# Optimization experiments

Hardware: AMD Instinct MI355X
Metric: run time of the kernel (lower is better)

## Reference

```python
import jax, jax.numpy as jnp
import numpy as np

N = 50000
E = 800000
IN_FEATS = 128
OUT_FEATS = 64
ALPHA = 0.2  # LeakyReLU negative slope


def setup_inputs() -> dict:
    key = jax.random.key(0)
    k1, k2, k3, k4, k5 = jax.random.split(key, 5)
    h = jax.random.normal(k1, (N, IN_FEATS), dtype=jnp.float32)
    src = jax.random.randint(k2, (E,), 0, N)
    dst = jax.random.randint(k3, (E,), 0, N)
    edge_index = jnp.stack([src, dst], axis=0).astype(jnp.int64)
    # xavier_uniform with gain=1.414
    limW = 1.414 * np.sqrt(6.0 / (IN_FEATS + OUT_FEATS))
    W = jax.random.uniform(k4, (IN_FEATS, OUT_FEATS), dtype=jnp.float32, minval=-limW, maxval=limW)
    lima = 1.414 * np.sqrt(6.0 / (2 * OUT_FEATS + 1))
    a = jax.random.uniform(k5, (2 * OUT_FEATS, 1), dtype=jnp.float32, minval=-lima, maxval=lima)
    return {"h": h, "edge_index": edge_index, "W": W, "a": a}


def reference(h, edge_index, W, a):
    src, dst = edge_index[0], edge_index[1]
    Wh = h @ W                               # (N, out)
    # split attention vector: cat([Wh_src, Wh_dst]) @ a == Wh_src@a1 + Wh_dst@a2
    a1 = a[:OUT_FEATS, 0]                    # (out,)
    a2 = a[OUT_FEATS:, 0]                    # (out,)
    s1 = Wh @ a1                             # (N,)
    s2 = Wh @ a2                             # (N,)
    e = jax.nn.leaky_relu(s1[src] + s2[dst], negative_slope=ALPHA)  # (E,)
    exp_e = jnp.exp(e)
    denom = jax.ops.segment_sum(exp_e, dst, num_segments=N)          # (N,)
    attention = exp_e / denom[dst]                                   # (E,)
    # dropout p=0.0 / eval mode -> identity
    msgs = attention[:, None] * Wh[src]                              # (E, out)
    h_prime = jax.ops.segment_sum(msgs, dst, num_segments=N)         # (N, out)
    return jax.nn.elu(h_prime)
```

## Files before the change

kernel.cpp:

```cpp
#include <hip/hip_runtime.h>
#include <math.h>

#define GN 50000
#define GE 800000
#define INF 128
#define OUTF 64
#define LRELU_ALPHA 0.2f

#define BUCK_SH 6
#define BUCKW   64
#define NB      ((GN + BUCKW - 1) / BUCKW)
#define CHUNK   4096
#define NCH     ((GE + CHUNK - 1) / CHUNK)
#define CAP     1536

__device__ __forceinline__ unsigned short f32_to_bf16(float f) {
    unsigned int u = __float_as_uint(f);
    return (unsigned short)((u + 0x7fffu + ((u >> 16) & 1u)) >> 16);
}
__device__ __forceinline__ float bf16lo(unsigned int u) { return __uint_as_float(u << 16); }
__device__ __forceinline__ float bf16hi(unsigned int u) { return __uint_as_float(u & 0xffff0000u); }

__global__ __launch_bounds__(256) void k_gemm(const float* __restrict__ h,
                                              const float* __restrict__ W,
                                              const float* __restrict__ a,
                                              unsigned short* __restrict__ Whb,
                                              float* __restrict__ s1,
                                              float* __restrict__ s2,
                                              int* __restrict__ cursor) {
    __shared__ __align__(16) float Wlds[INF * OUTF];
    int t = threadIdx.x;
    if (t == 0) cursor[blockIdx.x] = blockIdx.x * CAP;
    for (int i = t * 4; i < INF * OUTF; i += 256 * 4)
        *(float4*)&Wlds[i] = *(const float4*)&W[i];
    __syncthreads();

    int fg = t & 15;
    int ng = t >> 4;
    int jg = fg * 4;
    int n0 = blockIdx.x * 64 + ng * 4;

    int m0 = n0 + 0 < GN ? n0 + 0 : GN - 1;
    int m1 = n0 + 1 < GN ? n0 + 1 : GN - 1;
    int m2 = n0 + 2 < GN ? n0 + 2 : GN - 1;
    int m3 = n0 + 3 < GN ? n0 + 3 : GN - 1;
    const float* h0 = &h[m0 * INF];
    const float* h1 = &h[m1 * INF];
    const float* h2 = &h[m2 * INF];
    const float* h3 = &h[m3 * INF];

    float4 acc0 = {0.f,0.f,0.f,0.f}, acc1 = acc0, acc2 = acc0, acc3 = acc0;
    for (int kc = 0; kc < INF; kc += 4) {
        float4 hv0 = *(const float4*)&h0[kc];
        float4 hv1 = *(const float4*)&h1[kc];
        float4 hv2 = *(const float4*)&h2[kc];
        float4 hv3 = *(const float4*)&h3[kc];
        #pragma unroll
        for (int kk = 0; kk < 4; ++kk) {
            float4 wv = *(float4*)&Wlds[(kc + kk) * OUTF + jg];
            float a0 = ((const float*)&hv0)[kk];
            float a1v = ((const float*)&hv1)[kk];
            float a2v = ((const float*)&hv2)[kk];
            float a3 = ((const float*)&hv3)[kk];
            acc0.x += a0 * wv.x; acc0.y += a0 * wv.y; acc0.z += a0 * wv.z; acc0.w += a0 * wv.w;
            acc1.x += a1v * wv.x; acc1.y += a1v * wv.y; acc1.z += a1v * wv.z; acc1.w += a1v * wv.w;
            acc2.x += a2v * wv.x; acc2.y += a2v * wv.y; acc2.z += a2v * wv.z; acc2.w += a2v * wv.w;
            acc3.x += a3 * wv.x; acc3.y += a3 * wv.y; acc3.z += a3 * wv.z; acc3.w += a3 * wv.w;
        }
    }

    float4 accs[4] = {acc0, acc1, acc2, acc3};
    #pragma unroll
    for (int i = 0; i < 4; ++i) {
        if (n0 + i < GN) {
            ushort4 p;
            p.x = f32_to_bf16(accs[i].x); p.y = f32_to_bf16(accs[i].y);
            p.z = f32_to_bf16(accs[i].z); p.w = f32_to_bf16(accs[i].w);
            *(ushort4*)&Whb[(n0 + i) * OUTF + jg] = p;
        }
    }

    float4 va1 = *(const float4*)&a[jg];
    float4 va2 = *(const float4*)&a[OUTF + jg];
    float p1[4], p2[4];
    #pragma unroll
    for (int i = 0; i < 4; ++i) {
        p1[i] = accs[i].x * va1.x + accs[i].y * va1.y + accs[i].z * va1.z + accs[i].w * va1.w;
        p2[i] = accs[i].x * va2.x + accs[i].y * va2.y + accs[i].z * va2.z + accs[i].w * va2.w;
    }
    #pragma unroll
    for (int off = 8; off >= 1; off >>= 1) {
        #pragma unroll
        for (int i = 0; i < 4; ++i) {
            p1[i] += __shfl_down(p1[i], off, 16);
            p2[i] += __shfl_down(p2[i], off, 16);
        }
    }
    if (fg == 0) {
        #pragma unroll
        for (int i = 0; i < 4; ++i) {
            if (n0 + i < GN) { s1[n0 + i] = p1[i]; s2[n0 + i] = p2[i]; }
        }
    }
}

__global__ __launch_bounds__(256) void k_mscatter(const int* __restrict__ src,
                                                  const int* __restrict__ dst,
                                                  int* __restrict__ cursor,
                                                  int* __restrict__ epacked) {
    __shared__ int hist[NB];
    __shared__ int run[NB];
    int t = threadIdx.x;
    for (int i = t; i < NB; i += 256) hist[i] = 0;
    __syncthreads();

    int base = blockIdx.x * CHUNK;
    int pk[CHUNK / 256];
    int bb[CHUNK / 256];
    #pragma unroll
    for (int i = 0; i < CHUNK / 256; ++i) {
        int e = base + i * 256 + t;
        if (e < GE) {
            int d = dst[e];
            int b = d >> BUCK_SH;
            pk[i] = (src[e] << BUCK_SH) | (d & (BUCKW - 1));
            bb[i] = b;
            atomicAdd(&hist[b], 1);
        } else {
            bb[i] = -1;
        }
    }
    __syncthreads();
    for (int i = t; i < NB; i += 256) {
        int c = hist[i];
        if (c > 0) run[i] = atomicAdd(&cursor[i], c);
    }
    __syncthreads();
    #pragma unroll
    for (int i = 0; i < CHUNK / 256; ++i) {
        if (bb[i] >= 0) {
            int pos = atomicAdd(&run[bb[i]], 1);
            epacked[pos] = pk[i];
        }
    }
}

__global__ __launch_bounds__(256) void k_fgather(const int* __restrict__ cursor,
                                                 const int* __restrict__ epacked,
                                                 const float* __restrict__ s1,
                                                 const float* __restrict__ s2,
                                                 const unsigned short* __restrict__ Whb,
                                                 float* __restrict__ out) {
    __shared__ int elds[CAP];
    __shared__ int sorted[CAP];
    __shared__ int hist[BUCKW];
    __shared__ int cur[BUCKW];
    __shared__ int cstart[BUCKW + 1];
    __shared__ float s2l[BUCKW];

    int t = threadIdx.x;
    int b = blockIdx.x;
    int dstbase = b * BUCKW;
    int nd = GN - dstbase; if (nd > BUCKW) nd = BUCKW;

    int start = b * CAP;
    int cnt   = cursor[b] - start;
    if (cnt > CAP) cnt = CAP;

    if (t < BUCKW) {
        hist[t] = 0;
        s2l[t] = (t < nd) ? s2[dstbase + t] : 0.f;
    }
    __syncthreads();
    for (int i = t; i < cnt; i += 256) {
        int pk = epacked[start + i];
        elds[i] = pk;
        atomicAdd(&hist[pk & (BUCKW - 1)], 1);
    }
    __syncthreads();
    if (t < 64) {
        int v = hist[t];
        int incl = v;
        #pragma unroll
        for (int off = 1; off < 64; off <<= 1) {
            int u = __shfl_up(incl, off, 64);
            if (t >= off) incl += u;
        }
        cstart[t + 1] = incl;
        cur[t] = incl - v;
        if (t == 0) cstart[0] = 0;
    }
    __syncthreads();
    for (int i = t; i < cnt; i += 256) {
        int pk = elds[i];
        int pos = atomicAdd(&cur[pk & (BUCKW - 1)], 1);
        sorted[pos] = pk;
    }
    __syncthreads();

    int grp  = t >> 3;
    int lane = t & 7;
    int jg   = lane * 8;
    for (int dl = grp; dl < BUCKW; dl += 32) {
        int c0 = cstart[dl], c1 = cstart[dl + 1];
        float acc[8] = {0.f,0.f,0.f,0.f,0.f,0.f,0.f,0.f};
        float den = 0.f;
        float s2n = s2l[dl];
        for (int cb = c0; cb < c1; cb += 8) {
            int my = cb + lane;
            float ex_l = 0.f; int s_l = 0;
            if (my < c1) {
                int pk = sorted[my];
                s_l = pk >> BUCK_SH;
                float x = s1[s_l] + s2n;
                x = (x > 0.f) ? x : LRELU_ALPHA * x;
                ex_l = expf(x);
            }
            int m = c1 - cb; if (m > 8) m = 8;
            int   sj[8]; float exj[8];
            #pragma unroll
            for (int j = 0; j < 8; ++j) {
                exj[j] = __shfl(ex_l, j, 8);
                sj[j]  = __shfl(s_l,  j, 8);
            }
            uint4 wv[8];
            #pragma unroll
            for (int j = 0; j < 8; ++j)
                if (j < m) wv[j] = *(const uint4*)&Whb[sj[j] * OUTF + jg];
            #pragma unroll
            for (int j = 0; j < 8; ++j) {
                if (j < m) {
                    float ex = exj[j];
                    den += ex;
                    acc[0] += ex * bf16lo(wv[j].x); acc[1] += ex * bf16hi(wv[j].x);
                    acc[2] += ex * bf16lo(wv[j].y); acc[3] += ex * bf16hi(wv[j].y);
                    acc[4] += ex * bf16lo(wv[j].z); acc[5] += ex * bf16hi(wv[j].z);
                    acc[6] += ex * bf16lo(wv[j].w); acc[7] += ex * bf16hi(wv[j].w);
                }
            }
        }
        if (dl < nd) {
            float inv = (c1 > c0) ? 1.f / den : 0.f;
            float o[8];
            #pragma unroll
            for (int j = 0; j < 8; ++j) {
                float v = acc[j] * inv;
                o[j] = (v > 0.f) ? v : expm1f(v);
            }
            float* op = &out[(dstbase + dl) * OUTF + jg];
            *(float4*)(op + 0) = make_float4(o[0], o[1], o[2], o[3]);
            *(float4*)(op + 4) = make_float4(o[4], o[5], o[6], o[7]);
        }
    }
}

extern "C" void kernel_launch(void* const* d_in, const int* in_sizes, int n_in,
                              void* d_out, int out_size, void* d_ws, size_t ws_size,
                              hipStream_t stream) {
    const float* h  = (const float*)d_in[0];
    const int*   ei = (const int*)d_in[1];
    const float* W  = (const float*)d_in[2];
    const float* a  = (const float*)d_in[3];
    const int* src = ei;
    const int* dst = ei + GE;

    float* ws = (float*)d_ws;
    float* s1 = ws;
    float* s2 = s1 + GN;
    unsigned short* Whb = (unsigned short*)(s2 + GN);
    int* epacked = (int*)(Whb + (size_t)GN * OUTF);
    int* cursor  = epacked + (size_t)NB * CAP;
    float* out = (float*)d_out;

    k_gemm<<<NB, 256, 0, stream>>>(h, W, a, Whb, s1, s2, cursor);
    k_mscatter<<<NCH, 256, 0, stream>>>(src, dst, cursor, epacked);
    k_fgather<<<NB, 256, 0, stream>>>(cursor, epacked, s1, s2, Whb, out);
}
```

Before: 140.5 us.

## Merge GEMM and edge bucket-scatter into one launch with per-bucket counters

Combines the dense projection kernel and the edge bucketing scatter into one grid, where the first NB blocks compute Wh and the attention scores and the rest bucket edges by destination. This lets the two independent phases run concurrently on the GPU and removes one kernel launch boundary. The per-bucket cursor becomes a zero-initialized count set by a memset, since the GEMM blocks can no longer initialize it before the scatter runs. The cost is an extra memset node, and the block-to-role split may leave the device unevenly loaded.

```diff
diff --git a/kernel.cpp b/kernel.cpp
--- a/kernel.cpp
+++ b/kernel.cpp
@@ -21,131 +21,130 @@
 __device__ __forceinline__ float bf16lo(unsigned int u) { return __uint_as_float(u << 16); }
 __device__ __forceinline__ float bf16hi(unsigned int u) { return __uint_as_float(u & 0xffff0000u); }
 
-__global__ __launch_bounds__(256) void k_gemm(const float* __restrict__ h,
-                                              const float* __restrict__ W,
-                                              const float* __restrict__ a,
-                                              unsigned short* __restrict__ Whb,
-                                              float* __restrict__ s1,
-                                              float* __restrict__ s2,
-                                              int* __restrict__ cursor) {
+__global__ __launch_bounds__(256) void k_front(const float* __restrict__ h,
+                                               const float* __restrict__ W,
+                                               const float* __restrict__ a,
+                                               const int* __restrict__ src,
+                                               const int* __restrict__ dst,
+                                               unsigned short* __restrict__ Whb,
+                                               float* __restrict__ s1,
+                                               float* __restrict__ s2,
+                                               int* __restrict__ ccount,
+                                               int* __restrict__ epacked) {
     __shared__ __align__(16) float Wlds[INF * OUTF];
     int t = threadIdx.x;
-    if (t == 0) cursor[blockIdx.x] = blockIdx.x * CAP;
-    for (int i = t * 4; i < INF * OUTF; i += 256 * 4)
-        *(float4*)&Wlds[i] = *(const float4*)&W[i];
-    __syncthreads();
-
-    int fg = t & 15;
-    int ng = t >> 4;
-    int jg = fg * 4;
-    int n0 = blockIdx.x * 64 + ng * 4;
-
-    int m0 = n0 + 0 < GN ? n0 + 0 : GN - 1;
-    int m1 = n0 + 1 < GN ? n0 + 1 : GN - 1;
-    int m2 = n0 + 2 < GN ? n0 + 2 : GN - 1;
-    int m3 = n0 + 3 < GN ? n0 + 3 : GN - 1;
-    const float* h0 = &h[m0 * INF];
-    const float* h1 = &h[m1 * INF];
-    const float* h2 = &h[m2 * INF];
-    const float* h3 = &h[m3 * INF];
-
-    float4 acc0 = {0.f,0.f,0.f,0.f}, acc1 = acc0, acc2 = acc0, acc3 = acc0;
-    for (int kc = 0; kc < INF; kc += 4) {
-        float4 hv0 = *(const float4*)&h0[kc];
-        float4 hv1 = *(const float4*)&h1[kc];
-        float4 hv2 = *(const float4*)&h2[kc];
-        float4 hv3 = *(const float4*)&h3[kc];
-        #pragma unroll
-        for (int kk = 0; kk < 4; ++kk) {
-            float4 wv = *(float4*)&Wlds[(kc + kk) * OUTF + jg];
-            float a0 = ((const float*)&hv0)[kk];
-            float a1v = ((const float*)&hv1)[kk];
-            float a2v = ((const float*)&hv2)[kk];
-            float a3 = ((const float*)&hv3)[kk];
-            acc0.x += a0 * wv.x; acc0.y += a0 * wv.y; acc0.z += a0 * wv.z; acc0.w += a0 * wv.w;
-            acc1.x += a1v * wv.x; acc1.y += a1v * wv.y; acc1.z += a1v * wv.z; acc1.w += a1v * wv.w;
-            acc2.x += a2v * wv.x; acc2.y += a2v * wv.y; acc2.z += a2v * wv.z; acc2.w += a2v * wv.w;
-            acc3.x += a3 * wv.x; acc3.y += a3 * wv.y; acc3.z += a3 * wv.z; acc3.w += a3 * wv.w;
-        }
-    }
-
-    float4 accs[4] = {acc0, acc1, acc2, acc3};
-    #pragma unroll
-    for (int i = 0; i < 4; ++i) {
-        if (n0 + i < GN) {
-            ushort4 p;
-            p.x = f32_to_bf16(accs[i].x); p.y = f32_to_bf16(accs[i].y);
-            p.z = f32_to_bf16(accs[i].z); p.w = f32_to_bf16(accs[i].w);
-            *(ushort4*)&Whb[(n0 + i) * OUTF + jg] = p;
-        }
-    }
-
-    float4 va1 = *(const float4*)&a[jg];
-    float4 va2 = *(const float4*)&a[OUTF + jg];
-    float p1[4], p2[4];
-    #pragma unroll
-    for (int i = 0; i < 4; ++i) {
-        p1[i] = accs[i].x * va1.x + accs[i].y * va1.y + accs[i].z * va1.z + accs[i].w * va1.w;
-        p2[i] = accs[i].x * va2.x + accs[i].y * va2.y + accs[i].z * va2.z + accs[i].w * va2.w;
-    }
-    #pragma unroll
-    for (int off = 8; off >= 1; off >>= 1) {
+
+    if (blockIdx.x < NB) {
+        for (int i = t * 4; i < INF * OUTF; i += 256 * 4)
+            *(float4*)&Wlds[i] = *(const float4*)&W[i];
+        __syncthreads();
+
+        int fg = t & 15;
+        int ng = t >> 4;
+        int jg = fg * 4;
+        int n0 = blockIdx.x * 64 + ng * 4;
+
+        int m0 = n0 + 0 < GN ? n0 + 0 : GN - 1;
+        int m1 = n0 + 1 < GN ? n0 + 1 : GN - 1;
+        int m2 = n0 + 2 < GN ? n0 + 2 : GN - 1;
+        int m3 = n0 + 3 < GN ? n0 + 3 : GN - 1;
+        const float* h0 = &h[m0 * INF];
+        const float* h1 = &h[m1 * INF];
+        const float* h2 = &h[m2 * INF];
+        const float* h3 = &h[m3 * INF];
+
+        float4 acc0 = {0.f,0.f,0.f,0.f}, acc1 = acc0, acc2 = acc0, acc3 = acc0;
+        for (int kc = 0; kc < INF; kc += 4) {
+            float4 hv0 = *(const float4*)&h0[kc];
+            float4 hv1 = *(const float4*)&h1[kc];
+            float4 hv2 = *(const float4*)&h2[kc];
+            float4 hv3 = *(const float4*)&h3[kc];
+            #pragma unroll
+            for (int kk = 0; kk < 4; ++kk) {
+                float4 wv = *(float4*)&Wlds[(kc + kk) * OUTF + jg];
+                float a0 = ((const float*)&hv0)[kk];
+                float a1v = ((const float*)&hv1)[kk];
+                float a2v = ((const float*)&hv2)[kk];
+                float a3 = ((const float*)&hv3)[kk];
+                acc0.x += a0 * wv.x; acc0.y += a0 * wv.y; acc0.z += a0 * wv.z; acc0.w += a0 * wv.w;
+                acc1.x += a1v * wv.x; acc1.y += a1v * wv.y; acc1.z += a1v * wv.z; acc1.w += a1v * wv.w;
+                acc2.x += a2v * wv.x; acc2.y += a2v * wv.y; acc2.z += a2v * wv.z; acc2.w += a2v * wv.w;
+                acc3.x += a3 * wv.x; acc3.y += a3 * wv.y; acc3.z += a3 * wv.z; acc3.w += a3 * wv.w;
+            }
+        }
+
+        float4 accs[4] = {acc0, acc1, acc2, acc3};
         #pragma unroll
         for (int i = 0; i < 4; ++i) {
-            p1[i] += __shfl_down(p1[i], off, 16);
-            p2[i] += __shfl_down(p2[i], off, 16);
-        }
-    }
-    if (fg == 0) {
+            if (n0 + i < GN) {
+                ushort4 p;
+                p.x = f32_to_bf16(accs[i].x); p.y = f32_to_bf16(accs[i].y);
+                p.z = f32_to_bf16(accs[i].z); p.w = f32_to_bf16(accs[i].w);
+                *(ushort4*)&Whb[(n0 + i) * OUTF + jg] = p;
+            }
+        }
+
+        float4 va1 = *(const float4*)&a[jg];
+        float4 va2 = *(const float4*)&a[OUTF + jg];
+        float p1[4], p2[4];
         #pragma unroll
         for (int i = 0; i < 4; ++i) {
-            if (n0 + i < GN) { s1[n0 + i] = p1[i]; s2[n0 + i] = p2[i]; }
-        }
-    }
-}
-
-__global__ __launch_bounds__(256) void k_mscatter(const int* __restrict__ src,
-                                                  const int* __restrict__ dst,
-                                                  int* __restrict__ cursor,
-                                                  int* __restrict__ epacked) {
-    __shared__ int hist[NB];
-    __shared__ int run[NB];
-    int t = threadIdx.x;
-    for (int i = t; i < NB; i += 256) hist[i] = 0;
-    __syncthreads();
-
-    int base = blockIdx.x * CHUNK;
-    int pk[CHUNK / 256];
-    int bb[CHUNK / 256];
-    #pragma unroll
-    for (int i = 0; i < CHUNK / 256; ++i) {
-        int e = base + i * 256 + t;
-        if (e < GE) {
-            int d = dst[e];
-            int b = d >> BUCK_SH;
-            pk[i] = (src[e] << BUCK_SH) | (d & (BUCKW - 1));
-            bb[i] = b;
-            atomicAdd(&hist[b], 1);
-        } else {
-            bb[i] = -1;
-        }
-    }
-    __syncthreads();
-    for (int i = t; i < NB; i += 256) {
-        int c = hist[i];
-        if (c > 0) run[i] = atomicAdd(&cursor[i], c);
-    }
-    __syncthreads();
-    #pragma unroll
-    for (int i = 0; i < CHUNK / 256; ++i) {
-        if (bb[i] >= 0) {
-            int pos = atomicAdd(&run[bb[i]], 1);
-            epacked[pos] = pk[i];
-        }
-    }
-}
-
-__global__ __launch_bounds__(256) void k_fgather(const int* __restrict__ cursor,
+            p1[i] = accs[i].x * va1.x + accs[i].y * va1.y + accs[i].z * va1.z + accs[i].w * va1.w;
+            p2[i] = accs[i].x * va2.x + accs[i].y * va2.y + accs[i].z * va2.z + accs[i].w * va2.w;
+        }
+        #pragma unroll
+        for (int off = 8; off >= 1; off >>= 1) {
+            #pragma unroll
+            for (int i = 0; i < 4; ++i) {
+                p1[i] += __shfl_down(p1[i], off, 16);
+                p2[i] += __shfl_down(p2[i], off, 16);
+            }
+        }
+        if (fg == 0) {
+            #pragma unroll
+            for (int i = 0; i < 4; ++i) {
+                if (n0 + i < GN) { s1[n0 + i] = p1[i]; s2[n0 + i] = p2[i]; }
+            }
+        }
+    } else {
+        int* hist = (int*)Wlds;
+        int* run  = hist + NB;
+        for (int i = t; i < NB; i += 256) hist[i] = 0;
+        __syncthreads();
+
+        int base = (blockIdx.x - NB) * CHUNK;
+        int pk[CHUNK / 256];
+        int bb[CHUNK / 256];
+        #pragma unroll
+        for (int i = 0; i < CHUNK / 256; ++i) {
+            int e = base + i * 256 + t;
+            if (e < GE) {
+                int d = dst[e];
+                int b = d >> BUCK_SH;
+                pk[i] = (src[e] << BUCK_SH) | (d & (BUCKW - 1));
+                bb[i] = b;
+                atomicAdd(&hist[b], 1);
+            } else {
+                bb[i] = -1;
+            }
+        }
+        __syncthreads();
+        for (int i = t; i < NB; i += 256) {
+            int c = hist[i];
+            if (c > 0) run[i] = i * CAP + atomicAdd(&ccount[i], c);
+        }
+        __syncthreads();
+        #pragma unroll
+        for (int i = 0; i < CHUNK / 256; ++i) {
+            if (bb[i] >= 0) {
+                int pos = atomicAdd(&run[bb[i]], 1);
+                epacked[pos] = pk[i];
+            }
+        }
+    }
+}
+
+__global__ __launch_bounds__(256) void k_fgather(const int* __restrict__ ccount,
                                                  const int* __restrict__ epacked,
                                                  const float* __restrict__ s1,
                                                  const float* __restrict__ s2,
@@ -164,7 +163,7 @@
     int nd = GN - dstbase; if (nd > BUCKW) nd = BUCKW;
 
     int start = b * CAP;
-    int cnt   = cursor[b] - start;
+    int cnt   = ccount[b];
     if (cnt > CAP) cnt = CAP;
 
     if (t < BUCKW) {
@@ -269,10 +268,11 @@
     float* s2 = s1 + GN;
     unsigned short* Whb = (unsigned short*)(s2 + GN);
     int* epacked = (int*)(Whb + (size_t)GN * OUTF);
-    int* cursor  = epacked + (size_t)NB * CAP;
+    int* ccount  = epacked + (size_t)NB * CAP;
     float* out = (float*)d_out;
 
-    k_gemm<<<NB, 256, 0, stream>>>(h, W, a, Whb, s1, s2, cursor);
-    k_mscatter<<<NCH, 256, 0, stream>>>(src, dst, cursor, epacked);
-    k_fgather<<<NB, 256, 0, stream>>>(cursor, epacked, s1, s2, Whb, out);
-}
+    hipMemsetAsync(ccount, 0, NB * sizeof(int), stream);
+    k_front<<<NB + NCH, 256, 0, stream>>>(h, W, a, src, dst, Whb, s1, s2,
+                                          ccount, epacked);
+    k_fgather<<<NB, 256, 0, stream>>>(ccount, epacked, s1, s2, Whb, out);
+}
```

New measurement: 131.1 us. 6.7% less time.
